# Performance work log

Hardware: AMD Instinct MI355X
Metric: run time of the kernel (lower is better)

## Reference

```python
import jax, jax.numpy as jnp
import numpy as np
from math import ceil

CAPACITY_FACTOR = 2.0
MIN_CAPACITY = 4


def setup_inputs() -> dict:
    key = jax.random.key(0)
    ks = jax.random.split(key, 4)
    B, S, D, Di, E = 4, 2048, 1024, 4096, 8
    x = jax.random.normal(ks[0], (B, S, D), dtype=jnp.float32)
    Wr = jax.random.normal(ks[1], (D, E), dtype=jnp.float32) * (D ** -0.5)
    W1 = jax.random.normal(ks[2], (E, D, Di), dtype=jnp.float32) * (D ** -0.5)
    b1 = jnp.zeros((E, Di), dtype=jnp.float32)
    W2 = jax.random.normal(ks[3], (E, Di, D), dtype=jnp.float32) * (Di ** -0.5)
    b2 = jnp.zeros((E, D), dtype=jnp.float32)
    return {"x": x, "Wr": Wr, "W1": W1, "b1": b1, "W2": W2, "b2": b2}


def reference(x, Wr, W1, b1, W2, b2):
    B, S, D = x.shape
    E = Wr.shape[1]
    N = B * S
    k = max(MIN_CAPACITY, ceil(N * CAPACITY_FACTOR / E))  # expert capacity (static)

    xt = x.reshape(N, D)
    scores = jax.nn.softmax(xt @ Wr, axis=-1)          # [N, E] router probs
    G, idx = jax.lax.top_k(scores.T, k)                 # [E, k]: each expert picks top-k tokens

    # dispatch: equivalent to P @ x with P = one_hot(idx, N)
    X_in = xt[idx]                                      # [E, k, D]

    # per-expert MLP (batched over experts): Linear -> GELU(exact) -> Linear
    h = jax.nn.gelu(jnp.einsum('ekd,edh->ekh', X_in, W1) + b1[:, None, :], approximate=False)
    X_e = jnp.einsum('ekh,ehd->ekd', h, W2) + b2[:, None, :]  # [E, k, D]

    # combine: einsum('ijl,ij,ijd->ld', P, G, X_e) == scatter-add of G*X_e at idx
    contrib = (G[..., None] * X_e).reshape(E * k, D)
    out = jnp.zeros((N, D), dtype=x.dtype).at[idx.reshape(-1)].add(contrib)
    return out.reshape(B, S, D)
```

## Files before the change

### kernel.cpp

```cpp
#include <hip/hip_runtime.h>
#include <hip/hip_bf16.h>
#include <cstdint>
#include <cstddef>

#define NTOK 8192
#define DMODEL 1024
#define DFF 4096
#define NEXP 8
#define CAP 2048

typedef __attribute__((ext_vector_type(8))) __bf16 bf16x8;
typedef __attribute__((ext_vector_type(4))) float f32x4;

__device__ __forceinline__ void gload16(const void* g, void* l) {
  __builtin_amdgcn_global_load_lds(
      (__attribute__((address_space(1))) void*)(g),
      (__attribute__((address_space(3))) void*)(l),
      16, 0, 0);
}
#define VMWAIT_(n) asm volatile("s_waitcnt vmcnt(" #n ")" ::: "memory")
#define VMWAIT(n) VMWAIT_(n)
#define MEMFENCE asm volatile("" ::: "memory")

__global__ __launch_bounds__(256) void zero_f32(float* p, int n4) {
  int i = blockIdx.x * blockDim.x + threadIdx.x;
  int stride = gridDim.x * blockDim.x;
  float4 z = make_float4(0.f, 0.f, 0.f, 0.f);
  for (; i < n4; i += stride) ((float4*)p)[i] = z;
}

__global__ __launch_bounds__(256) void router_kernel(
    const float* __restrict__ x, const float* __restrict__ Wr,
    float* __restrict__ scoresT, __hip_bfloat16* __restrict__ xb) {
  const int lane = threadIdx.x & 63;
  const int t = blockIdx.x * 4 + (threadIdx.x >> 6);
  const float* xr = x + (size_t)t * DMODEL;
  float acc[NEXP];
#pragma unroll
  for (int j = 0; j < NEXP; ++j) acc[j] = 0.f;
#pragma unroll
  for (int it = 0; it < DMODEL / 64; ++it) {
    int d = it * 64 + lane;
    float xv = xr[d];
    xb[(size_t)t * DMODEL + d] = __float2bfloat16(xv);
    const float4* w = (const float4*)(Wr + (size_t)d * NEXP);
    float4 w0 = w[0], w1 = w[1];
    acc[0] += xv * w0.x; acc[1] += xv * w0.y; acc[2] += xv * w0.z; acc[3] += xv * w0.w;
    acc[4] += xv * w1.x; acc[5] += xv * w1.y; acc[6] += xv * w1.z; acc[7] += xv * w1.w;
  }
#pragma unroll
  for (int off = 32; off; off >>= 1) {
#pragma unroll
    for (int j = 0; j < NEXP; ++j) acc[j] += __shfl_xor(acc[j], off);
  }
  float m = acc[0];
#pragma unroll
  for (int j = 1; j < NEXP; ++j) m = fmaxf(m, acc[j]);
  float s = 0.f;
#pragma unroll
  for (int j = 0; j < NEXP; ++j) { acc[j] = expf(acc[j] - m); s += acc[j]; }
  float inv = 1.f / s;
  if (lane < NEXP) scoresT[(size_t)lane * NTOK + t] = acc[lane] * inv;
}

__global__ __launch_bounds__(256) void topk_kernel(
    const float* __restrict__ scoresT, float* __restrict__ G, int* __restrict__ IDX) {
  __shared__ uint32_t sb[NTOK];
  __shared__ uint32_t hist[256];
  __shared__ uint32_t s_prefix, s_rem;
  __shared__ uint32_t eq_list[256];
  __shared__ uint32_t eq_cnt, gt_cnt;
  const int e = blockIdx.x, tid = threadIdx.x;
  const float* se = scoresT + (size_t)e * NTOK;
  for (int i = tid; i < NTOK; i += 256) sb[i] = __float_as_uint(se[i]);
  if (tid == 0) { s_prefix = 0u; s_rem = CAP; eq_cnt = 0u; gt_cnt = 0u; }
  __syncthreads();
  for (int r = 0; r < 4; ++r) {
    const int shift = 24 - 8 * r;
    for (int i = tid; i < 256; i += 256) hist[i] = 0u;
    __syncthreads();
    uint32_t pfx = s_prefix;
    for (int i = tid; i < NTOK; i += 256) {
      uint32_t b = sb[i];
      if (((b >> shift) >> 8) == pfx) atomicAdd(&hist[(b >> shift) & 255u], 1u);
    }
    __syncthreads();
    if (tid == 0) {
      uint32_t rem = s_rem, cum = 0u;
      int d = 255;
      for (; d > 0; --d) {
        if (cum + hist[d] >= rem) break;
        cum += hist[d];
      }
      s_prefix = (pfx << 8) | (uint32_t)d;
      s_rem = rem - cum;
    }
    __syncthreads();
  }
  const uint32_t T = s_prefix, need = s_rem;
  for (int i = tid; i < NTOK; i += 256) {
    uint32_t b = sb[i];
    if (b > T) {
      uint32_t p = atomicAdd(&gt_cnt, 1u);
      IDX[(size_t)e * CAP + p] = i;
      G[(size_t)e * CAP + p] = __uint_as_float(b);
    } else if (b == T) {
      uint32_t c = atomicAdd(&eq_cnt, 1u);
      if (c < 256u) eq_list[c] = (uint32_t)i;
    }
  }
  __syncthreads();
  if (tid == 0) {
    uint32_t base = gt_cnt;
    uint32_t c = eq_cnt < 256u ? eq_cnt : 256u;
    for (uint32_t s = 0; s < need; ++s) {
      uint32_t mv = 0xFFFFFFFFu; int mi = 0;
      for (uint32_t j = 0; j < c; ++j)
        if (eq_list[j] < mv) { mv = eq_list[j]; mi = (int)j; }
      eq_list[mi] = 0xFFFFFFFFu;
      IDX[(size_t)e * CAP + base + s] = (int)mv;
      G[(size_t)e * CAP + base + s] = __uint_as_float(T);
    }
  }
}

__global__ __launch_bounds__(256) void transpose_cvt(
    const float* __restrict__ in, __hip_bfloat16* __restrict__ out, int R, int C) {
  __shared__ float tile[32][33];
  const int e = blockIdx.z;
  const float* ine = in + (size_t)e * R * C;
  __hip_bfloat16* oute = out + (size_t)e * R * C;
  const int c0 = blockIdx.x * 32, r0 = blockIdx.y * 32;
  const int tx = threadIdx.x, ty = threadIdx.y;
#pragma unroll
  for (int i = 0; i < 4; ++i)
    tile[ty + i * 8][tx] = ine[(size_t)(r0 + ty + i * 8) * C + (c0 + tx)];
  __syncthreads();
  const int rp = (tx & 15) * 2;
#pragma unroll
  for (int i = 0; i < 2; ++i) {
    int cl = ty + (tx >> 4) * 8 + i * 16;
    __hip_bfloat16 a = __float2bfloat16(tile[rp][cl]);
    __hip_bfloat16 b = __float2bfloat16(tile[rp + 1][cl]);
    ushort2 v = make_ushort2(*(unsigned short*)&a, *(unsigned short*)&b);
    *(ushort2*)(&oute[(size_t)(c0 + cl) * R + (r0 + rp)]) = v;
  }
}


#define RD_A(BASE, H)                                                          \
  {                                                                            \
    _Pragma("unroll") for (int mi = 0; mi < 4; ++mi)                           \
        _Pragma("unroll") for (int ks = 0; ks < 2; ++ks) av[mi][ks] =          \
        *(const bf16x8*)((BASE) + Ab + offA[(H)*4 + mi][ks]);                  \
  }
#define RD_B(BASE, BV, H2)                                                     \
  {                                                                            \
    _Pragma("unroll") for (int ni = 0; ni < 2; ++ni)                           \
        _Pragma("unroll") for (int ks = 0; ks < 2; ++ks) BV[ni][ks] =          \
        *(const bf16x8*)((BASE) + Bb + offB[(H2)*2 + ni][ks]);                 \
  }
#define STAGE_A(H, BUF)                                                        \
  {                                                                            \
    gload16(pa[(H)*2], (BUF) + (H)*16384 + dst);                               \
    pa[(H)*2] += 128;                                                          \
    gload16(pa[(H)*2 + 1], (BUF) + (H)*16384 + 8192 + dst);                    \
    pa[(H)*2 + 1] += 128;                                                      \
  }
#define STAGE_B(H, BUF)                                                        \
  {                                                                            \
    gload16(pb[(H)*2], (BUF) + 32768 + (H)*16384 + dst);                       \
    pb[(H)*2] += 128;                                                          \
    gload16(pb[(H)*2 + 1], (BUF) + 32768 + (H)*16384 + 8192 + dst);            \
    pb[(H)*2 + 1] += 128;                                                      \
  }
#define PH_PRE                                                                 \
  __builtin_amdgcn_s_barrier();                                                \
  MEMFENCE;                                                                    \
  asm volatile("s_waitcnt lgkmcnt(0)" ::: "memory");                           \
  __builtin_amdgcn_sched_barrier(0);                                           \
  __builtin_amdgcn_s_setprio(1);
#define PH_POST __builtin_amdgcn_s_setprio(0);
#define MFMA_Q(MB, NB, BV)                                                     \
  {                                                                            \
    _Pragma("unroll") for (int mi = 0; mi < 4; ++mi)                           \
        _Pragma("unroll") for (int ni = 0; ni < 2; ++ni)                       \
            _Pragma("unroll") for (int ks = 0; ks < 2; ++ks)                   \
                acc[(MB) + mi][(NB) + ni] =                                    \
        __builtin_amdgcn_mfma_f32_16x16x32_bf16(                               \
            av[mi][ks], BV[ni][ks], acc[(MB) + mi][(NB) + ni], 0, 0, 0);       \
  }

template <int NKT>
__device__ __forceinline__ void gemm_core8(
    const char* pa0, const char* pa1, const char* pa2, const char* pa3,
    const char* pb0, const char* pb1, const char* pb2, const char* pb3,
    char* smem, f32x4 (&acc)[8][4]) {
  const int tid = threadIdx.x;
  const int wave = tid >> 6, lane = tid & 63;
  const int wm = wave >> 2, wn = wave & 3;
  const int lrow = lane & 15, lgrp = lane >> 4;
  const int dst = tid * 16;

  const char* pa[4] = {pa0, pa1, pa2, pa3};
  const char* pb[4] = {pb0, pb1, pb2, pb3};

  int offA[8][2], offB[4][2];
#pragma unroll
  for (int mi = 0; mi < 8; ++mi) {
    int rL = mi * 16 + lrow;
#pragma unroll
    for (int ks = 0; ks < 2; ++ks)
      offA[mi][ks] = rL * 128 + ((((ks * 4 + lgrp) + rL) & 7) << 4);
  }
#pragma unroll
  for (int ni = 0; ni < 4; ++ni) {
    int rL = (wn & 1) * 64 + ni * 16 + lrow;
#pragma unroll
    for (int ks = 0; ks < 2; ++ks)
      offB[ni][ks] = rL * 128 + ((((ks * 4 + lgrp) + rL) & 7) << 4);
  }
  const int Ab = wm * 16384;
  const int Bb = 32768 + (wn >> 1) * 16384;

  char* b0 = smem;
  char* b1 = smem + 65536;

#pragma unroll
  for (int g = 0; g < 4; ++g) {
    gload16(pa[g], b0 + (g >> 1) * 16384 + (g & 1) * 8192 + dst);
    pa[g] += 128;
  }
#pragma unroll
  for (int g = 0; g < 4; ++g) {
    gload16(pb[g], b0 + 32768 + (g >> 1) * 16384 + (g & 1) * 8192 + dst);
    pb[g] += 128;
  }
#pragma unroll
  for (int g = 0; g < 4; ++g) {
    gload16(pb[g], b1 + 32768 + (g >> 1) * 16384 + (g & 1) * 8192 + dst);
    pb[g] += 128;
  }
  VMWAIT(4);
  __builtin_amdgcn_s_barrier();
  MEMFENCE;

  bf16x8 av[4][2], bv0[2][2], bv1[2][2];

  for (int i = 0; i < NKT / 2; ++i) {
    const bool st2 = (2 * i + 2 < NKT);
    const bool st3 = (2 * i + 3 < NKT);

    RD_A(b0, 0); RD_B(b0, bv0, 0);
    STAGE_A(0, b1);
    PH_PRE; MFMA_Q(0, 0, bv0); PH_POST;
    RD_B(b0, bv1, 1);
    STAGE_A(1, b1);
    PH_PRE; MFMA_Q(0, 2, bv1); PH_POST;
    RD_A(b0, 1);
    if (st2) STAGE_B(0, b0);
    PH_PRE; MFMA_Q(4, 2, bv1); PH_POST;
    if (st2) STAGE_B(1, b0);
    PH_PRE; MFMA_Q(4, 0, bv0);
    __builtin_amdgcn_s_setprio(0);
    if (st2) { VMWAIT(4); } else { VMWAIT(0); }
    __builtin_amdgcn_s_barrier();
    MEMFENCE;

    RD_A(b1, 0); RD_B(b1, bv0, 0);
    if (st2) STAGE_A(0, b0);
    PH_PRE; MFMA_Q(0, 0, bv0); PH_POST;
    RD_B(b1, bv1, 1);
    if (st2) STAGE_A(1, b0);
    PH_PRE; MFMA_Q(0, 2, bv1); PH_POST;
    RD_A(b1, 1);
    if (st3) STAGE_B(0, b1);
    PH_PRE; MFMA_Q(4, 2, bv1); PH_POST;
    if (st3) STAGE_B(1, b1);
    PH_PRE; MFMA_Q(4, 0, bv0);
    __builtin_amdgcn_s_setprio(0);
    if (st3) { VMWAIT(4); }
    __builtin_amdgcn_s_barrier();
    MEMFENCE;
  }
}

__device__ __forceinline__ float gelu_tanh(float v) {
  float t = 0.7978845608028654f * (v + 0.044715f * v * v * v);
  float e = __expf(2.f * t);
  float th = 1.f - 2.f / (e + 1.f);
  return 0.5f * v * (1.f + th);
}

__global__ __launch_bounds__(512, 2) void gemm1_kernel(
    const __hip_bfloat16* __restrict__ xb,
    const __hip_bfloat16* __restrict__ W1t,
    const float* __restrict__ b1,
    const int* __restrict__ IDX,
    __hip_bfloat16* __restrict__ h, int e0, int nblk) {
  __shared__ __align__(16) char smem[131072];
  int lin = blockIdx.x;
  { int q = nblk >> 3; lin = (lin & 7) * q + (lin >> 3); }
  const int tm = lin & 7, tn = (lin >> 3) & 15, ez = lin >> 7;
  const int e = e0 + ez;
  const int tid = threadIdx.x, wave = tid >> 6, lane = tid & 63;
  const int wm = wave >> 2, wn = wave & 3;
  const int lrow = lane & 15, lgrp = lane >> 4;

  const int r0 = tid >> 3;
  const int ksrc = (((tid & 7) - r0) & 7) * 16;
  const char* pa[4]; const char* pb[4];
#pragma unroll
  for (int g = 0; g < 4; ++g) {
    int m = g * 64 + r0;
    int tok = IDX[e * CAP + tm * 256 + m];
    pa[g] = (const char*)(xb + (size_t)tok * DMODEL) + ksrc;
    int n = g * 64 + r0;
    pb[g] = (const char*)(W1t + ((size_t)e * DFF + tn * 256 + n) * DMODEL) + ksrc;
  }

  f32x4 acc[8][4];
  f32x4 zero = {0.f, 0.f, 0.f, 0.f};
#pragma unroll
  for (int mi = 0; mi < 8; ++mi)
#pragma unroll
    for (int ni = 0; ni < 4; ++ni) acc[mi][ni] = zero;

  gemm_core8<DMODEL / 64>(pa[0], pa[1], pa[2], pa[3],
                          pb[0], pb[1], pb[2], pb[3], smem, acc);

  __hip_bfloat16* he = h + (size_t)ez * CAP * DFF;
  const float* b1e = b1 + (size_t)e * DFF;
  float bvals[4];
#pragma unroll
  for (int ni = 0; ni < 4; ++ni)
    bvals[ni] = b1e[tn * 256 + wn * 64 + ni * 16 + lrow];
  char* sb = smem;
  const int wswz = lgrp << 5;
#pragma unroll
  for (int mi = 0; mi < 8; ++mi) {
#pragma unroll
    for (int j = 0; j < 4; ++j) {
      int row = wm * 128 + mi * 16 + lgrp * 4 + j;
#pragma unroll
      for (int ni = 0; ni < 4; ++ni) {
        int col = wn * 64 + ni * 16 + lrow;
        float v = acc[mi][ni][j] + bvals[ni];
        v = gelu_tanh(v);
        *(__hip_bfloat16*)(sb + ((row * 512 + col * 2) ^ wswz)) =
            __float2bfloat16(v);
      }
    }
  }
  __syncthreads();
  size_t obase = (size_t)(tm * 256) * DFF + tn * 256;
#pragma unroll
  for (int c = 0; c < 16; ++c) {
    int byte = c * 8192 + tid * 16;
    int row = byte >> 9;
    int rswz = ((row >> 2) & 3) << 5;
    bf16x8 vals = *(const bf16x8*)(sb + (byte ^ rswz));
    int col = (byte & 511) >> 1;
    *(bf16x8*)(he + obase + (size_t)row * DFF + col) = vals;
  }
}

__global__ __launch_bounds__(512, 2) void gemm2_kernel(
    const __hip_bfloat16* __restrict__ h,
    const __hip_bfloat16* __restrict__ W2t,
    const float* __restrict__ b2,
    const int* __restrict__ IDX, const float* __restrict__ G,
    float* __restrict__ out, int e0, int nblk) {
  __shared__ __align__(16) char smem[131072];
  int lin = blockIdx.x;
  { int q = nblk >> 3; lin = (lin & 7) * q + (lin >> 3); }
  const int tm = lin & 7, tn = (lin >> 3) & 3, ez = lin >> 5;
  const int e = e0 + ez;
  const int tid = threadIdx.x, wave = tid >> 6, lane = tid & 63;
  const int wm = wave >> 2, wn = wave & 3;
  const int lrow = lane & 15, lgrp = lane >> 4;

  const int r0 = tid >> 3;
  const int ksrc = (((tid & 7) - r0) & 7) * 16;
  const char* pa[4]; const char* pb[4];
#pragma unroll
  for (int g = 0; g < 4; ++g) {
    int m = g * 64 + r0;
    pa[g] = (const char*)(h + ((size_t)ez * CAP + tm * 256 + m) * DFF) + ksrc;
    int n = g * 64 + r0;
    pb[g] = (const char*)(W2t + ((size_t)e * DMODEL + tn * 256 + n) * DFF) + ksrc;
  }

  f32x4 acc[8][4];
  f32x4 zero = {0.f, 0.f, 0.f, 0.f};
#pragma unroll
  for (int mi = 0; mi < 8; ++mi)
#pragma unroll
    for (int ni = 0; ni < 4; ++ni) acc[mi][ni] = zero;

  gemm_core8<DFF / 64>(pa[0], pa[1], pa[2], pa[3],
                       pb[0], pb[1], pb[2], pb[3], smem, acc);

  const float* b2e = b2 + (size_t)e * DMODEL;
  const int* idxe = IDX + (size_t)e * CAP;
  const float* ge = G + (size_t)e * CAP;
  float bvals[4];
#pragma unroll
  for (int ni = 0; ni < 4; ++ni)
    bvals[ni] = b2e[tn * 256 + wn * 64 + ni * 16 + lrow];
#pragma unroll
  for (int mi = 0; mi < 8; ++mi) {
#pragma unroll
    for (int j = 0; j < 4; ++j) {
      int row = tm * 256 + wm * 128 + mi * 16 + lgrp * 4 + j;
      float g = ge[row];
      int tok = idxe[row];
      float* orow = out + (size_t)tok * DMODEL;
#pragma unroll
      for (int ni = 0; ni < 4; ++ni) {
        int col = tn * 256 + wn * 64 + ni * 16 + lrow;
        atomicAdd(orow + col, (acc[mi][ni][j] + bvals[ni]) * g);
      }
    }
  }
}

extern "C" void kernel_launch(void* const* d_in, const int* in_sizes, int n_in,
                              void* d_out, int out_size, void* d_ws, size_t ws_size,
                              hipStream_t stream) {
  const float* x  = (const float*)d_in[0];
  const float* Wr = (const float*)d_in[1];
  const float* W1 = (const float*)d_in[2];
  const float* b1 = (const float*)d_in[3];
  const float* W2 = (const float*)d_in[4];
  const float* b2 = (const float*)d_in[5];
  float* out = (float*)d_out;
  char* ws = (char*)d_ws;

  size_t off = 0;
  float* scoresT = (float*)(ws + off); off += (size_t)NEXP * NTOK * 4;
  float* G       = (float*)(ws + off); off += (size_t)NEXP * CAP * 4;
  int*   IDX     = (int*)(ws + off);   off += (size_t)NEXP * CAP * 4;
  __hip_bfloat16* xb  = (__hip_bfloat16*)(ws + off); off += (size_t)NTOK * DMODEL * 2;
  __hip_bfloat16* W1t = (__hip_bfloat16*)(ws + off); off += (size_t)NEXP * DFF * DMODEL * 2;
  __hip_bfloat16* W2t = (__hip_bfloat16*)(ws + off); off += (size_t)NEXP * DMODEL * DFF * 2;
  __hip_bfloat16* hbuf = (__hip_bfloat16*)(ws + off);
  size_t h_per_e = (size_t)CAP * DFF * 2;
  size_t avail = (ws_size > off) ? (ws_size - off) : 0;
  int EC = (int)(avail / h_per_e);
  if (EC < 1) EC = 1;
  if (EC > NEXP) EC = NEXP;

  zero_f32<<<512, 256, 0, stream>>>(out, out_size / 4);
  router_kernel<<<NTOK / 4, 256, 0, stream>>>(x, Wr, scoresT, xb);
  topk_kernel<<<NEXP, 256, 0, stream>>>(scoresT, G, IDX);
  transpose_cvt<<<dim3(DFF / 32, DMODEL / 32, NEXP), dim3(32, 8), 0, stream>>>(
      W1, W1t, DMODEL, DFF);
  transpose_cvt<<<dim3(DMODEL / 32, DFF / 32, NEXP), dim3(32, 8), 0, stream>>>(
      W2, W2t, DFF, DMODEL);
  for (int e0 = 0; e0 < NEXP; e0 += EC) {
    int ne = (NEXP - e0 < EC) ? (NEXP - e0) : EC;
    int nblk1 = 128 * ne;
    gemm1_kernel<<<nblk1, 512, 0, stream>>>(xb, W1t, b1, IDX, hbuf, e0, nblk1);
    int nblk2 = 32 * ne;
    gemm2_kernel<<<nblk2, 512, 0, stream>>>(hbuf, W2t, b2, IDX, G, out, e0, nblk2);
  }
}
```

Before: 475.4 us.

## Replace atomic scatter combine with gather via inverse index, tile transpose 64x64, parallel topk scan

The gemm2 epilogue now writes gate-scaled expert outputs as bf16 into a dense Xe buffer, staged through swizzled shared memory, instead of issuing fp32 atomicAdds into the output. A new build_inv kernel records, for each token, which expert slots picked it, and a combine_kernel gathers and sums those rows, writing each output row once, so the full output zeroing is no longer needed. Separately, the weight transpose/convert kernel moves to 64x64 tiles with float4 loads and 32-byte stores, and topk's serial single-thread histogram scan becomes a parallel suffix sum. The trade-off is an extra bf16 round-trip of expert outputs through memory and rounding of the combined values to bf16 before summation.

```diff
diff --git a/kernel.cpp b/kernel.cpp
--- a/kernel.cpp
+++ b/kernel.cpp
@@ -67,6 +67,7 @@
     const float* __restrict__ scoresT, float* __restrict__ G, int* __restrict__ IDX) {
   __shared__ uint32_t sb[NTOK];
   __shared__ uint32_t hist[256];
+  __shared__ uint32_t sfx[256];
   __shared__ uint32_t s_prefix, s_rem;
   __shared__ uint32_t eq_list[256];
   __shared__ uint32_t eq_cnt, gt_cnt;
@@ -77,7 +78,7 @@
   __syncthreads();
   for (int r = 0; r < 4; ++r) {
     const int shift = 24 - 8 * r;
-    for (int i = tid; i < 256; i += 256) hist[i] = 0u;
+    hist[tid] = 0u;
     __syncthreads();
     uint32_t pfx = s_prefix;
     for (int i = tid; i < NTOK; i += 256) {
@@ -85,15 +86,19 @@
       if (((b >> shift) >> 8) == pfx) atomicAdd(&hist[(b >> shift) & 255u], 1u);
     }
     __syncthreads();
-    if (tid == 0) {
-      uint32_t rem = s_rem, cum = 0u;
-      int d = 255;
-      for (; d > 0; --d) {
-        if (cum + hist[d] >= rem) break;
-        cum += hist[d];
-      }
-      s_prefix = (pfx << 8) | (uint32_t)d;
-      s_rem = rem - cum;
+    sfx[tid] = hist[tid];
+    __syncthreads();
+#pragma unroll
+    for (int off = 1; off < 256; off <<= 1) {
+      uint32_t v = sfx[tid] + ((tid + off < 256) ? sfx[tid + off] : 0u);
+      __syncthreads();
+      sfx[tid] = v;
+      __syncthreads();
+    }
+    uint32_t rem = s_rem;
+    if (sfx[tid] >= rem && (tid == 255 || sfx[tid + 1] < rem)) {
+      s_prefix = (pfx << 8) | (uint32_t)tid;
+      s_rem = rem - ((tid == 255) ? 0u : sfx[tid + 1]);
     }
     __syncthreads();
   }
@@ -124,29 +129,66 @@
   }
 }
 
+__global__ __launch_bounds__(256) void build_inv(
+    const int* __restrict__ IDX, int* __restrict__ cnt, int* __restrict__ inv) {
+  int i = blockIdx.x * 256 + threadIdx.x;
+  int t = IDX[i];
+  int c = atomicAdd(&cnt[t], 1);
+  inv[t * 8 + c] = i;
+}
+
+__global__ __launch_bounds__(256) void combine_kernel(
+    const __hip_bfloat16* __restrict__ Xe, const int* __restrict__ inv,
+    const int* __restrict__ cnt, float* __restrict__ out) {
+  const int w = (blockIdx.x * 256 + threadIdx.x) >> 6;
+  const int lane = threadIdx.x & 63;
+  const int c = cnt[w];
+  float a[16];
+#pragma unroll
+  for (int i = 0; i < 16; ++i) a[i] = 0.f;
+  for (int j = 0; j < c; ++j) {
+    int s = inv[w * 8 + j];
+    const bf16x8* p = (const bf16x8*)(Xe + (size_t)s * DMODEL + lane * 16);
+    bf16x8 v0 = p[0], v1 = p[1];
+#pragma unroll
+    for (int i = 0; i < 8; ++i) {
+      a[i] += (float)v0[i];
+      a[8 + i] += (float)v1[i];
+    }
+  }
+  float4* o = (float4*)(out + (size_t)w * DMODEL + lane * 16);
+#pragma unroll
+  for (int q = 0; q < 4; ++q)
+    o[q] = make_float4(a[q * 4], a[q * 4 + 1], a[q * 4 + 2], a[q * 4 + 3]);
+}
+
 __global__ __launch_bounds__(256) void transpose_cvt(
     const float* __restrict__ in, __hip_bfloat16* __restrict__ out, int R, int C) {
-  __shared__ float tile[32][33];
+  __shared__ float tile[64][68];
   const int e = blockIdx.z;
   const float* ine = in + (size_t)e * R * C;
   __hip_bfloat16* oute = out + (size_t)e * R * C;
-  const int c0 = blockIdx.x * 32, r0 = blockIdx.y * 32;
-  const int tx = threadIdx.x, ty = threadIdx.y;
-#pragma unroll
-  for (int i = 0; i < 4; ++i)
-    tile[ty + i * 8][tx] = ine[(size_t)(r0 + ty + i * 8) * C + (c0 + tx)];
+  const int c0 = blockIdx.x * 64, r0 = blockIdx.y * 64;
+  const int tid = threadIdx.x;
+  const int lr = tid >> 4, lc = tid & 15;
+#pragma unroll
+  for (int it = 0; it < 4; ++it) {
+    int row = it * 16 + lr;
+    float4 v = *(const float4*)(ine + (size_t)(r0 + row) * C + c0 + lc * 4);
+    *(float4*)&tile[row][lc * 4] = v;
+  }
   __syncthreads();
-  const int rp = (tx & 15) * 2;
-#pragma unroll
-  for (int i = 0; i < 2; ++i) {
-    int cl = ty + (tx >> 4) * 8 + i * 16;
-    __hip_bfloat16 a = __float2bfloat16(tile[rp][cl]);
-    __hip_bfloat16 b = __float2bfloat16(tile[rp + 1][cl]);
-    ushort2 v = make_ushort2(*(unsigned short*)&a, *(unsigned short*)&b);
-    *(ushort2*)(&oute[(size_t)(c0 + cl) * R + (r0 + rp)]) = v;
-  }
-}
-
+  const int cc = tid >> 2, rq = tid & 3;
+  unsigned short pk[16];
+#pragma unroll
+  for (int i = 0; i < 16; ++i) {
+    __hip_bfloat16 b = __float2bfloat16(tile[rq * 16 + i][cc]);
+    pk[i] = *(unsigned short*)&b;
+  }
+  char* dst = (char*)(oute + (size_t)(c0 + cc) * R + r0 + rq * 16);
+  *(uint4*)dst = *(uint4*)&pk[0];
+  *(uint4*)(dst + 16) = *(uint4*)&pk[8];
+}
 
 #define RD_A(BASE, H)                                                          \
   {                                                                            \
@@ -254,12 +296,15 @@
     RD_A(b0, 0); RD_B(b0, bv0, 0);
     STAGE_A(0, b1);
     PH_PRE; MFMA_Q(0, 0, bv0); PH_POST;
+
     RD_B(b0, bv1, 1);
     STAGE_A(1, b1);
     PH_PRE; MFMA_Q(0, 2, bv1); PH_POST;
+
     RD_A(b0, 1);
     if (st2) STAGE_B(0, b0);
     PH_PRE; MFMA_Q(4, 2, bv1); PH_POST;
+
     if (st2) STAGE_B(1, b0);
     PH_PRE; MFMA_Q(4, 0, bv0);
     __builtin_amdgcn_s_setprio(0);
@@ -270,12 +315,15 @@
     RD_A(b1, 0); RD_B(b1, bv0, 0);
     if (st2) STAGE_A(0, b0);
     PH_PRE; MFMA_Q(0, 0, bv0); PH_POST;
+
     RD_B(b1, bv1, 1);
     if (st2) STAGE_A(1, b0);
     PH_PRE; MFMA_Q(0, 2, bv1); PH_POST;
+
     RD_A(b1, 1);
     if (st3) STAGE_B(0, b1);
     PH_PRE; MFMA_Q(4, 2, bv1); PH_POST;
+
     if (st3) STAGE_B(1, b1);
     PH_PRE; MFMA_Q(4, 0, bv0);
     __builtin_amdgcn_s_setprio(0);
@@ -369,8 +417,8 @@
     const __hip_bfloat16* __restrict__ h,
     const __hip_bfloat16* __restrict__ W2t,
     const float* __restrict__ b2,
-    const int* __restrict__ IDX, const float* __restrict__ G,
-    float* __restrict__ out, int e0, int nblk) {
+    const float* __restrict__ G,
+    __hip_bfloat16* __restrict__ Xe, int e0, int nblk) {
   __shared__ __align__(16) char smem[131072];
   int lin = blockIdx.x;
   { int q = nblk >> 3; lin = (lin & 7) * q + (lin >> 3); }
@@ -402,26 +450,38 @@
                        pb[0], pb[1], pb[2], pb[3], smem, acc);
 
   const float* b2e = b2 + (size_t)e * DMODEL;
-  const int* idxe = IDX + (size_t)e * CAP;
-  const float* ge = G + (size_t)e * CAP;
+  const float* ge = G + (size_t)e * CAP + tm * 256;
   float bvals[4];
 #pragma unroll
   for (int ni = 0; ni < 4; ++ni)
     bvals[ni] = b2e[tn * 256 + wn * 64 + ni * 16 + lrow];
+  char* sb = smem;
+  const int wswz = lgrp << 5;
 #pragma unroll
   for (int mi = 0; mi < 8; ++mi) {
 #pragma unroll
     for (int j = 0; j < 4; ++j) {
-      int row = tm * 256 + wm * 128 + mi * 16 + lgrp * 4 + j;
+      int row = wm * 128 + mi * 16 + lgrp * 4 + j;
       float g = ge[row];
-      int tok = idxe[row];
-      float* orow = out + (size_t)tok * DMODEL;
 #pragma unroll
       for (int ni = 0; ni < 4; ++ni) {
-        int col = tn * 256 + wn * 64 + ni * 16 + lrow;
-        atomicAdd(orow + col, (acc[mi][ni][j] + bvals[ni]) * g);
+        int col = wn * 64 + ni * 16 + lrow;
+        float v = (acc[mi][ni][j] + bvals[ni]) * g;
+        *(__hip_bfloat16*)(sb + ((row * 512 + col * 2) ^ wswz)) =
+            __float2bfloat16(v);
       }
     }
+  }
+  __syncthreads();
+  __hip_bfloat16* xbase = Xe + ((size_t)(e * CAP + tm * 256)) * DMODEL + tn * 256;
+#pragma unroll
+  for (int c = 0; c < 16; ++c) {
+    int byte = c * 8192 + tid * 16;
+    int row = byte >> 9;
+    int rswz = ((row >> 2) & 3) << 5;
+    bf16x8 vals = *(const bf16x8*)(sb + (byte ^ rswz));
+    int col = (byte & 511) >> 1;
+    *(bf16x8*)(xbase + (size_t)row * DMODEL + col) = vals;
   }
 }
 
@@ -441,9 +501,12 @@
   float* scoresT = (float*)(ws + off); off += (size_t)NEXP * NTOK * 4;
   float* G       = (float*)(ws + off); off += (size_t)NEXP * CAP * 4;
   int*   IDX     = (int*)(ws + off);   off += (size_t)NEXP * CAP * 4;
+  int*   cnt     = (int*)(ws + off);   off += (size_t)NTOK * 4;
+  int*   inv     = (int*)(ws + off);   off += (size_t)NTOK * 8 * 4;
   __hip_bfloat16* xb  = (__hip_bfloat16*)(ws + off); off += (size_t)NTOK * DMODEL * 2;
   __hip_bfloat16* W1t = (__hip_bfloat16*)(ws + off); off += (size_t)NEXP * DFF * DMODEL * 2;
   __hip_bfloat16* W2t = (__hip_bfloat16*)(ws + off); off += (size_t)NEXP * DMODEL * DFF * 2;
+  __hip_bfloat16* Xe  = (__hip_bfloat16*)(ws + off); off += (size_t)NEXP * CAP * DMODEL * 2;
   __hip_bfloat16* hbuf = (__hip_bfloat16*)(ws + off);
   size_t h_per_e = (size_t)CAP * DFF * 2;
   size_t avail = (ws_size > off) ? (ws_size - off) : 0;
@@ -451,18 +514,20 @@
   if (EC < 1) EC = 1;
   if (EC > NEXP) EC = NEXP;
 
-  zero_f32<<<512, 256, 0, stream>>>(out, out_size / 4);
+  zero_f32<<<8, 256, 0, stream>>>((float*)cnt, NTOK / 4);
   router_kernel<<<NTOK / 4, 256, 0, stream>>>(x, Wr, scoresT, xb);
   topk_kernel<<<NEXP, 256, 0, stream>>>(scoresT, G, IDX);
-  transpose_cvt<<<dim3(DFF / 32, DMODEL / 32, NEXP), dim3(32, 8), 0, stream>>>(
+  build_inv<<<NEXP * CAP / 256, 256, 0, stream>>>(IDX, cnt, inv);
+  transpose_cvt<<<dim3(DFF / 64, DMODEL / 64, NEXP), 256, 0, stream>>>(
       W1, W1t, DMODEL, DFF);
-  transpose_cvt<<<dim3(DMODEL / 32, DFF / 32, NEXP), dim3(32, 8), 0, stream>>>(
+  transpose_cvt<<<dim3(DMODEL / 64, DFF / 64, NEXP), 256, 0, stream>>>(
       W2, W2t, DFF, DMODEL);
   for (int e0 = 0; e0 < NEXP; e0 += EC) {
     int ne = (NEXP - e0 < EC) ? (NEXP - e0) : EC;
     int nblk1 = 128 * ne;
     gemm1_kernel<<<nblk1, 512, 0, stream>>>(xb, W1t, b1, IDX, hbuf, e0, nblk1);
     int nblk2 = 32 * ne;
-    gemm2_kernel<<<nblk2, 512, 0, stream>>>(hbuf, W2t, b2, IDX, G, out, e0, nblk2);
-  }
-}
+    gemm2_kernel<<<nblk2, 512, 0, stream>>>(hbuf, W2t, b2, G, Xe, e0, nblk2);
+  }
+  combine_kernel<<<NTOK / 4, 256, 0, stream>>>(Xe, inv, cnt, out);
+}
```

After: 413.6 us. 1.15x faster.
